# Kernel optimization log

Hardware: AMD Instinct MI355X
Metric: run time of the kernel (lower is better)

Reference implementation:

```python
import jax, jax.numpy as jnp
import numpy as np

B, S, D = 4, 2048, 1024
LN_EPS = 1e-3  # keras LayerNormalization default epsilon


def setup_inputs() -> dict:
    key = jax.random.key(0)
    ks = jax.random.split(key, 6)
    context = jax.random.normal(ks[0], (B, S, D), jnp.float32)
    eos_mask = jax.random.randint(ks[1], (B, 1, S, S), 0, 2).astype(jnp.int32)
    prior = jax.random.uniform(ks[2], (1,), jnp.float32)
    ln_gamma = jnp.ones((D,), jnp.float32)
    ln_beta = jnp.zeros((D,), jnp.float32)
    Wk = jax.random.normal(ks[3], (D, D), jnp.float32) / np.float32(np.sqrt(D))
    bk = jnp.zeros((D,), jnp.float32)
    Wq = jax.random.normal(ks[4], (D, D), jnp.float32) / np.float32(np.sqrt(D))
    bq = jnp.zeros((D,), jnp.float32)
    return dict(context=context, eos_mask=eos_mask, prior=prior,
                ln_gamma=ln_gamma, ln_beta=ln_beta, Wk=Wk, bk=bk, Wq=Wq, bq=bq)


def reference(context, eos_mask, prior, ln_gamma, ln_beta, Wk, bk, Wq, bq):
    seq_len = context.shape[1]
    d_model = jnp.float32(context.shape[-1])
    eos = jnp.squeeze(eos_mask, 1)  # [B,S,S]

    # LayerNorm over last axis
    mu = jnp.mean(context, axis=-1, keepdims=True)
    var = jnp.var(context, axis=-1, keepdims=True)
    x = (context - mu) * jax.lax.rsqrt(var + LN_EPS) * ln_gamma + ln_beta

    # constant band / triangular matrices
    a_mat = jnp.eye(seq_len, k=1, dtype=jnp.float32)
    b_mat = jnp.eye(seq_len, dtype=jnp.float32)
    c_mat = jnp.eye(seq_len, k=-1, dtype=jnp.float32)
    tri = jnp.triu(jnp.ones((seq_len, seq_len), jnp.float32))

    # mask: eos AND (super- or sub-diagonal)
    mask = ((eos != 0) & ((a_mat + c_mat) == 1.0)).astype(jnp.float32)

    k = x @ Wk + bk  # [B,S,D]
    q = x @ Wq + bq  # [B,S,D]
    scores = jnp.einsum('bqd,bkd->bqk', q, k) / d_model + mask * 1e-19
    neibor_attn = jax.nn.softmax(scores, axis=-1)
    neibor_attn = jnp.sqrt(jnp.square(neibor_attn + 1e-9))
    neibor_attn = prior + (1.0 - prior) * neibor_attn  # prior [1] broadcasts

    # log-domain cumulative (triangular) matmuls
    t_mat = jnp.einsum('bij,jk->bik', jnp.log(neibor_attn + 1e-9) * a_mat, tri)
    g_attn = jnp.exp(jnp.einsum('ij,bjk->bik', tri, t_mat)) * (tri - b_mat)
    g_attn = g_attn + jnp.transpose(g_attn, (0, 2, 1)) + (neibor_attn * b_mat + 1e-9)
    return (g_attn, neibor_attn)
```

## Files before the change

kernel.cpp:

```cpp
#include <hip/hip_runtime.h>

#define S_LEN 2048
#define D_MODEL 1024
#define NB 4

typedef unsigned short u16;
typedef __attribute__((ext_vector_type(8))) short short8;
typedef __attribute__((ext_vector_type(4))) float f32x4;
typedef __attribute__((ext_vector_type(4))) unsigned short u16x4;

__device__ inline u16 f2bf(float f) {
  union { float f; unsigned u; } v; v.f = f;
  unsigned u = v.u;
  unsigned r = (u + 0x7FFFu + ((u >> 16) & 1u)) >> 16;
  return (u16)r;
}

__device__ inline float bf2f(u16 b) {
  union { unsigned u; float f; } v; v.u = ((unsigned)b) << 16;
  return v.f;
}

__device__ inline void glds16(const void* g, void* l) {
  __builtin_amdgcn_global_load_lds((const __attribute__((address_space(1))) void*)g,
                                   (__attribute__((address_space(3))) void*)l,
                                   16, 0, 0);
}

__global__ __launch_bounds__(256) void w2_kernel(const float* __restrict__ Wk,
                                                 const float* __restrict__ bq,
                                                 float* __restrict__ w2) {
  const int r = blockIdx.x * 4 + (threadIdx.x >> 6);
  const int lane = threadIdx.x & 63;
  const f32x4* row = (const f32x4*)(Wk + (size_t)r * D_MODEL);
  float s = 0.0f;
  #pragma unroll
  for (int c = 0; c < 4; ++c) {
    const f32x4 v = row[lane * 4 + c];
    const f32x4 b = ((const f32x4*)bq)[lane * 4 + c];
    s += v[0]*b[0] + v[1]*b[1] + v[2]*b[2] + v[3]*b[3];
  }
  for (int o = 32; o > 0; o >>= 1) s += __shfl_xor(s, o);
  if (lane == 0) w2[r] = s;
}

__global__ __launch_bounds__(256) void ln_kernel(const float* __restrict__ ctx,
                                                 const float* __restrict__ gamma,
                                                 const float* __restrict__ beta,
                                                 const float* __restrict__ w2,
                                                 u16* __restrict__ xb,
                                                 float* __restrict__ bvec) {
  const int row = blockIdx.x;
  const int t = threadIdx.x;
  const f32x4 v = ((const f32x4*)(ctx + (size_t)row * D_MODEL))[t];
  float s = v[0] + v[1] + v[2] + v[3];
  float q = v[0]*v[0] + v[1]*v[1] + v[2]*v[2] + v[3]*v[3];
  for (int o = 32; o > 0; o >>= 1) { s += __shfl_xor(s, o); q += __shfl_xor(q, o); }
  __shared__ float rs[4], rq[4], rd[4];
  const int wave = t >> 6, lane = t & 63;
  if (lane == 0) { rs[wave] = s; rq[wave] = q; }
  __syncthreads();
  s = rs[0] + rs[1] + rs[2] + rs[3];
  q = rq[0] + rq[1] + rq[2] + rq[3];
  const float mu = s * (1.0f / D_MODEL);
  const float var = q * (1.0f / D_MODEL) - mu * mu;
  const float rstd = rsqrtf(var + 1e-3f);
  const f32x4 g4 = ((const f32x4*)gamma)[t];
  const f32x4 b4 = ((const f32x4*)beta)[t];
  const f32x4 w4 = ((const f32x4*)w2)[t];
  float xv[4];
  float dot = 0.0f;
  #pragma unroll
  for (int u = 0; u < 4; ++u) {
    xv[u] = (v[u] - mu) * rstd * g4[u] + b4[u];
    dot += xv[u] * w4[u];
  }
  u16x4 o;
  #pragma unroll
  for (int u = 0; u < 4; ++u) o[u] = f2bf(xv[u]);
  ((u16x4*)(xb + (size_t)row * D_MODEL))[t] = o;
  for (int of = 32; of > 0; of >>= 1) dot += __shfl_xor(dot, of);
  if (lane == 0) rd[wave] = dot;
  __syncthreads();
  if (t == 0) bvec[row] = (rd[0] + rd[1] + rd[2] + rd[3]) * (1.0f / D_MODEL);
}

__global__ __launch_bounds__(256) void prep_w(const float* __restrict__ Wq,
                                              const float* __restrict__ Wk,
                                              u16* __restrict__ Wt) {
  __shared__ float tile[32][33];
  const int k0 = blockIdx.x * 32;
  const int n0 = blockIdx.y * 32;
  const int tx = threadIdx.x, ty = threadIdx.y;
  const float* W = (n0 < D_MODEL) ? Wq : Wk;
  const int nl0 = (n0 < D_MODEL) ? n0 : (n0 - D_MODEL);
  #pragma unroll
  for (int j = 0; j < 32; j += 8)
    tile[ty + j][tx] = W[(size_t)(k0 + ty + j) * D_MODEL + nl0 + tx];
  __syncthreads();
  #pragma unroll
  for (int j = 0; j < 32; j += 8)
    Wt[(size_t)(n0 + ty + j) * D_MODEL + k0 + tx] = f2bf(tile[tx][ty + j]);
}

__global__ __launch_bounds__(256, 2) void gemm_bt(
    const u16* __restrict__ A, int lda, long long sA,
    const u16* __restrict__ Bt, int ldb, long long sB,
    u16* __restrict__ C, int ldc, long long sC,
    float scale, int K) {
  __shared__ u16 As[128][32];
  __shared__ u16 Bs[128][32];
  const int tid = threadIdx.x;
  const int wave = tid >> 6, lane = tid & 63;
  const int z = blockIdx.z;
  A += (size_t)z * sA;
  Bt += (size_t)z * sB;
  const size_t m0 = (size_t)blockIdx.y * 128;
  const size_t n0 = (size_t)blockIdx.x * 128;
  const int wr = (wave >> 1) * 64;
  const int wc = (wave & 1) * 64;
  const int strow = wave * 16 + (lane >> 2);
  const int stslot = (lane & 3) * 8;
  const int fr = lane & 15, fq = lane >> 4;

  f32x4 acc[4][4];
  #pragma unroll
  for (int i = 0; i < 4; ++i)
    #pragma unroll
    for (int j = 0; j < 4; ++j) acc[i][j] = (f32x4)(0.0f);

  for (int k0 = 0; k0 < K; k0 += 32) {
    const u16* ga = A + (m0 + strow) * lda + k0 + stslot;
    const u16* gb = Bt + (n0 + strow) * ldb + k0 + stslot;
    glds16(ga, &As[wave * 16][0]);
    glds16(ga + (size_t)64 * lda, &As[64 + wave * 16][0]);
    glds16(gb, &Bs[wave * 16][0]);
    glds16(gb + (size_t)64 * ldb, &Bs[64 + wave * 16][0]);
    __syncthreads();
    short8 af[4], bfv[4];
    #pragma unroll
    for (int mi = 0; mi < 4; ++mi) af[mi] = *(const short8*)&As[wr + mi * 16 + fr][fq * 8];
    #pragma unroll
    for (int ni = 0; ni < 4; ++ni) bfv[ni] = *(const short8*)&Bs[wc + ni * 16 + fr][fq * 8];
    #pragma unroll
    for (int mi = 0; mi < 4; ++mi)
      #pragma unroll
      for (int ni = 0; ni < 4; ++ni)
        acc[mi][ni] = __builtin_amdgcn_mfma_f32_16x16x32_bf16(af[mi], bfv[ni], acc[mi][ni], 0, 0, 0);
    __syncthreads();
  }

  #pragma unroll
  for (int mi = 0; mi < 4; ++mi)
    #pragma unroll
    for (int ni = 0; ni < 4; ++ni) {
      const size_t row = m0 + wr + mi * 16 + fq * 4;
      const size_t col = n0 + wc + ni * 16 + fr;
      #pragma unroll
      for (int r = 0; r < 4; ++r)
        C[((size_t)z * sC) + (row + r) * ldc + col] = f2bf(acc[mi][ni][r] * scale);
    }
}

__global__ __launch_bounds__(512, 2) void gemm8p256(
    const u16* __restrict__ A, int lda, long long sA,
    const u16* __restrict__ Bt, int ldb, long long sB,
    u16* __restrict__ C, int ldc, long long sC,
    float scale, int K) {
  __shared__ char smem[131072];
  const int tid = threadIdx.x;
  const int wave = tid >> 6, lane = tid & 63;
  const int fr = lane & 15, fq = lane >> 4;
  const int wm = wave >> 2, wn = wave & 3;
  const int z = blockIdx.z;
  const size_t m0 = (size_t)blockIdx.y * 256;
  const size_t n0 = (size_t)blockIdx.x * 256;
  const u16* Ab = A + (size_t)z * sA + m0 * lda;
  const u16* Bb = Bt + (size_t)z * sB + n0 * ldb;
  const int perA = (lane >> 3) * lda + (((lane & 7) ^ (lane >> 3)) * 8);
  const int perB = (lane >> 3) * ldb + (((lane & 7) ^ (lane >> 3)) * 8);
  const int u0v = wave * 2, u1v = wave * 2 + 1;
  const int rA_0 = (u0v & 7) * 8 + (u0v >> 3) * 128;
  const int rA_1 = (u1v & 7) * 8 + (u1v >> 3) * 128;
  const int rB_0 = (u0v >> 2) * 64 + (u0v & 3) * 8;
  const int rB_1 = (u1v >> 2) * 64 + (u1v & 3) * 8;
  const int sw0 = ((fq) ^ (fr & 7)) * 16;
  const int sw1 = ((4 + fq) ^ (fr & 7)) * 16;
  const int aBase = wm * 16384 + fr * 128;
  const int bBase = 32768 + wn * 8192 + fr * 128;

  f32x4 acc[8][4];
  #pragma unroll
  for (int i = 0; i < 8; ++i)
    #pragma unroll
    for (int j = 0; j < 4; ++j) acc[i][j] = (f32x4)(0.0f);

#define STG_A02(BUF, KK) do { \
    glds16(Ab + (size_t)rA_0 * lda + perA + (KK), smem + (BUF) + rA_0 * 128); \
    glds16(Ab + (size_t)rA_1 * lda + perA + (KK), smem + (BUF) + rA_1 * 128); } while (0)
#define STG_A13(BUF, KK) do { \
    glds16(Ab + (size_t)(rA_0 + 64) * lda + perA + (KK), smem + (BUF) + (rA_0 + 64) * 128); \
    glds16(Ab + (size_t)(rA_1 + 64) * lda + perA + (KK), smem + (BUF) + (rA_1 + 64) * 128); } while (0)
#define STG_BEV(BUF, KK) do { \
    glds16(Bb + (size_t)rB_0 * ldb + perB + (KK), smem + (BUF) + 32768 + rB_0 * 128); \
    glds16(Bb + (size_t)rB_1 * ldb + perB + (KK), smem + (BUF) + 32768 + rB_1 * 128); } while (0)
#define STG_BOD(BUF, KK) do { \
    glds16(Bb + (size_t)(rB_0 + 32) * ldb + perB + (KK), smem + (BUF) + 32768 + (rB_0 + 32) * 128); \
    glds16(Bb + (size_t)(rB_1 + 32) * ldb + perB + (KK), smem + (BUF) + 32768 + (rB_1 + 32) * 128); } while (0)

  const int NT = K >> 6;
  STG_A02(0, 0); STG_BEV(0, 0); STG_BOD(0, 0); STG_A13(0, 0);

  for (int t = 0; t < NT; ++t) {
    const int bo = (t & 1) * 65536;
    const int bn = bo ^ 65536;
    const int kk = (t + 1 < NT) ? (t + 1) * 64 : 0;
    short8 a0[8], a1[8], be[4], bod[4];

    asm volatile("s_waitcnt vmcnt(4)" ::: "memory");
    asm volatile("s_barrier" ::: "memory");
    #pragma unroll
    for (int fi = 0; fi < 4; ++fi) {
      a0[fi * 2 + 0] = *(const short8*)(smem + bo + aBase + fi * 2048 + sw0);
      a0[fi * 2 + 1] = *(const short8*)(smem + bo + aBase + fi * 2048 + sw1);
    }
    #pragma unroll
    for (int nj = 0; nj < 2; ++nj) {
      be[nj * 2 + 0] = *(const short8*)(smem + bo + bBase + nj * 2048 + sw0);
      be[nj * 2 + 1] = *(const short8*)(smem + bo + bBase + nj * 2048 + sw1);
    }
    STG_A02(bn, kk);
    __builtin_amdgcn_s_setprio(1);
    #pragma unroll
    for (int ks = 0; ks < 2; ++ks)
      #pragma unroll
      for (int fi = 0; fi < 4; ++fi)
        #pragma unroll
        for (int nj = 0; nj < 2; ++nj)
          acc[fi][nj] = __builtin_amdgcn_mfma_f32_16x16x32_bf16(a0[fi * 2 + ks], be[nj * 2 + ks], acc[fi][nj], 0, 0, 0);
    __builtin_amdgcn_s_setprio(0);

    asm volatile("s_waitcnt vmcnt(4)" ::: "memory");
    asm volatile("s_barrier" ::: "memory");
    #pragma unroll
    for (int nj = 0; nj < 2; ++nj) {
      bod[nj * 2 + 0] = *(const short8*)(smem + bo + bBase + 4096 + nj * 2048 + sw0);
      bod[nj * 2 + 1] = *(const short8*)(smem + bo + bBase + 4096 + nj * 2048 + sw1);
    }
    STG_BEV(bn, kk);
    __builtin_amdgcn_s_setprio(1);
    #pragma unroll
    for (int ks = 0; ks < 2; ++ks)
      #pragma unroll
      for (int fi = 0; fi < 4; ++fi)
        #pragma unroll
        for (int nj = 0; nj < 2; ++nj)
          acc[fi][2 + nj] = __builtin_amdgcn_mfma_f32_16x16x32_bf16(a0[fi * 2 + ks], bod[nj * 2 + ks], acc[fi][2 + nj], 0, 0, 0);
    __builtin_amdgcn_s_setprio(0);

    asm volatile("s_waitcnt vmcnt(4)" ::: "memory");
    asm volatile("s_barrier" ::: "memory");
    #pragma unroll
    for (int fi = 0; fi < 4; ++fi) {
      a1[fi * 2 + 0] = *(const short8*)(smem + bo + aBase + 8192 + fi * 2048 + sw0);
      a1[fi * 2 + 1] = *(const short8*)(smem + bo + aBase + 8192 + fi * 2048 + sw1);
    }
    STG_BOD(bn, kk);
    __builtin_amdgcn_s_setprio(1);
    #pragma unroll
    for (int ks = 0; ks < 2; ++ks)
      #pragma unroll
      for (int fi = 0; fi < 4; ++fi)
        #pragma unroll
        for (int nj = 0; nj < 2; ++nj)
          acc[4 + fi][nj] = __builtin_amdgcn_mfma_f32_16x16x32_bf16(a1[fi * 2 + ks], be[nj * 2 + ks], acc[4 + fi][nj], 0, 0, 0);
    __builtin_amdgcn_s_setprio(0);

    asm volatile("s_barrier" ::: "memory");
    STG_A13(bn, kk);
    __builtin_amdgcn_s_setprio(1);
    #pragma unroll
    for (int ks = 0; ks < 2; ++ks)
      #pragma unroll
      for (int fi = 0; fi < 4; ++fi)
        #pragma unroll
        for (int nj = 0; nj < 2; ++nj)
          acc[4 + fi][2 + nj] = __builtin_amdgcn_mfma_f32_16x16x32_bf16(a1[fi * 2 + ks], bod[nj * 2 + ks], acc[4 + fi][2 + nj], 0, 0, 0);
    __builtin_amdgcn_s_setprio(0);
  }
#undef STG_A02
#undef STG_A13
#undef STG_BEV
#undef STG_BOD

  u16* Cz = C + (size_t)z * sC;
  #pragma unroll
  for (int mi = 0; mi < 8; ++mi)
    #pragma unroll
    for (int ni = 0; ni < 4; ++ni) {
      const size_t row = m0 + wm * 128 + (mi >> 2) * 64 + (mi & 3) * 16 + fq * 4;
      const size_t col = n0 + wn * 64 + (ni >> 1) * 32 + (ni & 1) * 16 + fr;
      #pragma unroll
      for (int r = 0; r < 4; ++r)
        Cz[(row + r) * ldc + col] = f2bf(acc[mi][ni][r] * scale);
    }
}

__global__ __launch_bounds__(256) void softmax_kernel(const u16* __restrict__ Sb,
                                                      const float* __restrict__ bvec,
                                                      const float* __restrict__ prior,
                                                      float* __restrict__ na,
                                                      float* __restrict__ ell,
                                                      float* __restrict__ dvec) {
  const int row = blockIdx.x;
  const int t = threadIdx.x;
  const int b = row >> 11, i = row & (S_LEN - 1);
  const short8 sv = ((const short8*)(Sb + (size_t)row * S_LEN))[t];
  const f32x4 bv0 = ((const f32x4*)(bvec + (size_t)b * S_LEN))[t * 2];
  const f32x4 bv1 = ((const f32x4*)(bvec + (size_t)b * S_LEN))[t * 2 + 1];
  float v[8];
  #pragma unroll
  for (int u = 0; u < 8; ++u)
    v[u] = bf2f((u16)sv[u]) + ((u < 4) ? bv0[u] : bv1[u - 4]);
  float mx = v[0];
  #pragma unroll
  for (int u = 1; u < 8; ++u) mx = fmaxf(mx, v[u]);
  for (int o = 32; o > 0; o >>= 1) mx = fmaxf(mx, __shfl_xor(mx, o));
  __shared__ float red[4], red2[4];
  const int wave = t >> 6, lane = t & 63;
  if (lane == 0) red[wave] = mx;
  __syncthreads();
  mx = fmaxf(fmaxf(red[0], red[1]), fmaxf(red[2], red[3]));
  float e[8], s = 0.0f;
  #pragma unroll
  for (int u = 0; u < 8; ++u) { e[u] = __expf(v[u] - mx); s += e[u]; }
  for (int o = 32; o > 0; o >>= 1) s += __shfl_xor(s, o);
  if (lane == 0) red2[wave] = s;
  __syncthreads();
  s = red2[0] + red2[1] + red2[2] + red2[3];
  const float pr = prior[0];
  const float w = 1.0f - pr;
  const float inv = 1.0f / s;
  f32x4 o0, o1;
  #pragma unroll
  for (int u = 0; u < 4; ++u) o0[u] = pr + w * (e[u] * inv + 1e-9f);
  #pragma unroll
  for (int u = 0; u < 4; ++u) o1[u] = pr + w * (e[4 + u] * inv + 1e-9f);
  f32x4* nrow = (f32x4*)(na + (size_t)row * S_LEN);
  nrow[t * 2] = o0;
  nrow[t * 2 + 1] = o1;
  #pragma unroll
  for (int u = 0; u < 8; ++u) {
    const int j = t * 8 + u;
    const float ov = (u < 4) ? o0[u] : o1[u - 4];
    if (j == i) dvec[row] = ov;
    if (j == i + 1) ell[row] = logf(ov + 1e-9f);
  }
  if (i == S_LEN - 1 && t == 0) ell[row] = 0.0f;
}

__global__ __launch_bounds__(256) void scan_kernel(const float* __restrict__ ell,
                                                   float* __restrict__ Cpre) {
  const int b = blockIdx.x, t = threadIdx.x;
  const float* eb = ell + (size_t)b * S_LEN;
  const f32x4 e0 = ((const f32x4*)eb)[t * 2];
  const f32x4 e1 = ((const f32x4*)eb)[t * 2 + 1];
  float ev[8];
  #pragma unroll
  for (int u = 0; u < 4; ++u) ev[u] = e0[u];
  #pragma unroll
  for (int u = 0; u < 4; ++u) ev[4 + u] = e1[u];
  float loc[8], tot = 0.0f;
  #pragma unroll
  for (int u = 0; u < 8; ++u) { loc[u] = tot; tot += ev[u]; }
  __shared__ float sbuf[256];
  sbuf[t] = tot;
  __syncthreads();
  for (int off = 1; off < 256; off <<= 1) {
    const float v = (t >= off) ? sbuf[t - off] : 0.0f;
    __syncthreads();
    sbuf[t] += v;
    __syncthreads();
  }
  const float base = (t == 0) ? 0.0f : sbuf[t - 1];
  #pragma unroll
  for (int u = 0; u < 8; ++u)
    Cpre[(size_t)b * S_LEN + t * 8 + u] = base + loc[u];
}

__global__ __launch_bounds__(256) void gattn_kernel(const float* __restrict__ Cpre,
                                                    const float* __restrict__ dvec,
                                                    float* __restrict__ g) {
  const int b = blockIdx.z, i = blockIdx.y;
  const int j0 = blockIdx.x * 1024 + threadIdx.x * 4;
  const float Ci = Cpre[b * S_LEN + i];
  const float di = dvec[b * S_LEN + i];
  const f32x4 Cj = *(const f32x4*)&Cpre[b * S_LEN + j0];
  f32x4 o;
  #pragma unroll
  for (int u = 0; u < 4; ++u) {
    const int j = j0 + u;
    const float arg = (j > i) ? (Cj[u] - Ci) : (Ci - Cj[u]);
    o[u] = (j == i) ? (di + 1e-9f) : (__expf(arg) + 1e-9f);
  }
  *(f32x4*)(g + ((size_t)b * S_LEN + i) * S_LEN + j0) = o;
}

extern "C" void kernel_launch(void* const* d_in, const int* in_sizes, int n_in,
                              void* d_out, int out_size, void* d_ws, size_t ws_size,
                              hipStream_t stream) {
  const float* ctx   = (const float*)d_in[0];
  const float* prior = (const float*)d_in[2];
  const float* gamma = (const float*)d_in[3];
  const float* beta  = (const float*)d_in[4];
  const float* Wk    = (const float*)d_in[5];
  const float* Wq    = (const float*)d_in[7];
  const float* bq    = (const float*)d_in[8];

  float* g  = (float*)d_out;
  float* na = g + (size_t)NB * S_LEN * S_LEN;

  u16* Xb = (u16*)na;
  u16* Yb = Xb + (size_t)(NB * S_LEN) * D_MODEL;
  u16* PT = Yb + (size_t)(NB * S_LEN) * D_MODEL;
  u16* Wt = PT + (size_t)D_MODEL * D_MODEL;
  u16* Sb = (u16*)g;
  float* w2   = (float*)d_ws;
  float* bvec = w2 + D_MODEL;
  float* ell  = bvec + NB * S_LEN;
  float* dvec = ell + NB * S_LEN;
  float* Cpre = dvec + NB * S_LEN;

  w2_kernel<<<D_MODEL / 4, 256, 0, stream>>>(Wk, bq, w2);
  ln_kernel<<<NB * S_LEN, 256, 0, stream>>>(ctx, gamma, beta, w2, Xb, bvec);
  prep_w<<<dim3(32, 64), dim3(32, 8), 0, stream>>>(Wq, Wk, Wt);

  gemm_bt<<<dim3(8, 8, 1), 256, 0, stream>>>(Wt + (size_t)D_MODEL * D_MODEL, D_MODEL, 0,
                                             Wt, D_MODEL, 0,
                                             PT, D_MODEL, 0, 1.0f, D_MODEL);
  gemm_bt<<<dim3(8, 64, 1), 256, 0, stream>>>(Xb, D_MODEL, 0,
                                              PT, D_MODEL, 0,
                                              Yb, D_MODEL, 0, 1.0f, D_MODEL);
  gemm8p256<<<dim3(8, 8, NB), 512, 0, stream>>>(Yb, D_MODEL, (long long)S_LEN * D_MODEL,
                                                Xb, D_MODEL, (long long)S_LEN * D_MODEL,
                                                Sb, S_LEN, (long long)S_LEN * S_LEN,
                                                1.0f / (float)D_MODEL, D_MODEL);

  softmax_kernel<<<NB * S_LEN, 256, 0, stream>>>(Sb, bvec, prior, na, ell, dvec);
  scan_kernel<<<NB, 256, 0, stream>>>(ell, Cpre);
  gattn_kernel<<<dim3(2, S_LEN, NB), 256, 0, stream>>>(Cpre, dvec, g);
}
```

Baseline: 144.2 us.

## Run batched score GEMM in FP8 via scaled MFMA and tile the projection GEMM

The layer norm kernel now also writes an e4m3 FP8 copy of the normalized activations. The projection GEMM moves to a new 128x256 pipelined kernel that emits FP8 output. The large batched score GEMM becomes a new FP8 kernel built on the 32x32x64 scaled MFMA with 128-wide K steps. The goal is to halve operand bandwidth and raise matrix throughput in the dominant GEMM. The cost is lower precision in the scores, which the softmax and log/exp chain may amplify, and a fully drained vmcnt(0) wait each iteration.

```diff
diff --git a/kernel.cpp b/kernel.cpp
--- a/kernel.cpp
+++ b/kernel.cpp
@@ -1,4 +1,5 @@
 #include <hip/hip_runtime.h>
+#include <hip/hip_fp8.h>
 
 #define S_LEN 2048
 #define D_MODEL 1024
@@ -7,7 +8,10 @@
 typedef unsigned short u16;
 typedef __attribute__((ext_vector_type(8))) short short8;
 typedef __attribute__((ext_vector_type(4))) float f32x4;
+typedef __attribute__((ext_vector_type(16))) float f32x16;
 typedef __attribute__((ext_vector_type(4))) unsigned short u16x4;
+typedef __attribute__((ext_vector_type(4))) int i32x4;
+typedef __attribute__((ext_vector_type(8))) int i32x8;
 
 __device__ inline u16 f2bf(float f) {
   union { float f; unsigned u; } v; v.f = f;
@@ -21,10 +25,22 @@
   return v.f;
 }
 
+__device__ inline unsigned char f2e4m3(float f) {
+  __hip_fp8_e4m3 q(f);
+  return (unsigned char)q.__x;
+}
+
 __device__ inline void glds16(const void* g, void* l) {
   __builtin_amdgcn_global_load_lds((const __attribute__((address_space(1))) void*)g,
                                    (__attribute__((address_space(3))) void*)l,
                                    16, 0, 0);
+}
+
+__device__ inline i32x8 cat8(i32x4 a, i32x4 b) {
+  i32x8 r;
+  r[0] = a[0]; r[1] = a[1]; r[2] = a[2]; r[3] = a[3];
+  r[4] = b[0]; r[5] = b[1]; r[6] = b[2]; r[7] = b[3];
+  return r;
 }
 
 __global__ __launch_bounds__(256) void w2_kernel(const float* __restrict__ Wk,
@@ -49,6 +65,7 @@
                                                  const float* __restrict__ beta,
                                                  const float* __restrict__ w2,
                                                  u16* __restrict__ xb,
+                                                 unsigned char* __restrict__ x8,
                                                  float* __restrict__ bvec) {
   const int row = blockIdx.x;
   const int t = threadIdx.x;
@@ -79,6 +96,9 @@
   #pragma unroll
   for (int u = 0; u < 4; ++u) o[u] = f2bf(xv[u]);
   ((u16x4*)(xb + (size_t)row * D_MODEL))[t] = o;
+  unsigned pk = (unsigned)f2e4m3(xv[0]) | ((unsigned)f2e4m3(xv[1]) << 8) |
+                ((unsigned)f2e4m3(xv[2]) << 16) | ((unsigned)f2e4m3(xv[3]) << 24);
+  ((unsigned*)(x8 + (size_t)row * D_MODEL))[t] = pk;
   for (int of = 32; of > 0; of >>= 1) dot += __shfl_xor(dot, of);
   if (lane == 0) rd[wave] = dot;
   __syncthreads();
@@ -104,17 +124,14 @@
 }
 
 __global__ __launch_bounds__(256, 2) void gemm_bt(
-    const u16* __restrict__ A, int lda, long long sA,
-    const u16* __restrict__ Bt, int ldb, long long sB,
-    u16* __restrict__ C, int ldc, long long sC,
+    const u16* __restrict__ A, int lda,
+    const u16* __restrict__ Bt, int ldb,
+    u16* __restrict__ C, int ldc,
     float scale, int K) {
   __shared__ u16 As[128][32];
   __shared__ u16 Bs[128][32];
   const int tid = threadIdx.x;
   const int wave = tid >> 6, lane = tid & 63;
-  const int z = blockIdx.z;
-  A += (size_t)z * sA;
-  Bt += (size_t)z * sB;
   const size_t m0 = (size_t)blockIdx.y * 128;
   const size_t n0 = (size_t)blockIdx.x * 128;
   const int wr = (wave >> 1) * 64;
@@ -158,151 +175,232 @@
       const size_t col = n0 + wc + ni * 16 + fr;
       #pragma unroll
       for (int r = 0; r < 4; ++r)
-        C[((size_t)z * sC) + (row + r) * ldc + col] = f2bf(acc[mi][ni][r] * scale);
+        C[(row + r) * ldc + col] = f2bf(acc[mi][ni][r] * scale);
     }
 }
 
-__global__ __launch_bounds__(512, 2) void gemm8p256(
-    const u16* __restrict__ A, int lda, long long sA,
-    const u16* __restrict__ Bt, int ldb, long long sB,
+__global__ __launch_bounds__(512, 2) void gemm8p128(
+    const u16* __restrict__ A, int lda,
+    const u16* __restrict__ Bt, int ldb,
+    unsigned char* __restrict__ C8, int ldc,
+    float scale, int K) {
+  __shared__ char smem[98304];
+  const int tid = threadIdx.x;
+  const int wave = tid >> 6, lane = tid & 63;
+  const int fr = lane & 15, fq = lane >> 4;
+  const int wm = wave >> 2, wn = wave & 3;
+  const size_t m0 = (size_t)blockIdx.y * 128;
+  const size_t n0 = (size_t)blockIdx.x * 256;
+  const u16* Ab = A + m0 * lda;
+  const u16* Bb = Bt + n0 * ldb;
+  const int perA = (lane >> 3) * lda + (((lane & 7) ^ (lane >> 3)) * 8);
+  const int perB = (lane >> 3) * ldb + (((lane & 7) ^ (lane >> 3)) * 8);
+  const int u0v = wave * 2, u1v = wave * 2 + 1;
+  const int rA_0 = u0v * 8;
+  const int rA_1 = u1v * 8;
+  const int rB_0 = (u0v >> 2) * 64 + (u0v & 3) * 8;
+  const int rB_1 = (u1v >> 2) * 64 + (u1v & 3) * 8;
+  const int sw0 = ((fq) ^ (fr & 7)) * 16;
+  const int sw1 = ((4 + fq) ^ (fr & 7)) * 16;
+  const int aBase = wm * 8192 + fr * 128;
+  const int bBase = 16384 + wn * 8192 + fr * 128;
+
+  f32x4 acc[4][4];
+  #pragma unroll
+  for (int i = 0; i < 4; ++i)
+    #pragma unroll
+    for (int j = 0; j < 4; ++j) acc[i][j] = (f32x4)(0.0f);
+
+#define STG_A(BUF, KK) do { \
+    glds16(Ab + (size_t)rA_0 * lda + perA + (KK), smem + (BUF) + rA_0 * 128); \
+    glds16(Ab + (size_t)rA_1 * lda + perA + (KK), smem + (BUF) + rA_1 * 128); } while (0)
+#define STG_BEV(BUF, KK) do { \
+    glds16(Bb + (size_t)rB_0 * ldb + perB + (KK), smem + (BUF) + 16384 + rB_0 * 128); \
+    glds16(Bb + (size_t)rB_1 * ldb + perB + (KK), smem + (BUF) + 16384 + rB_1 * 128); } while (0)
+#define STG_BOD(BUF, KK) do { \
+    glds16(Bb + (size_t)(rB_0 + 32) * ldb + perB + (KK), smem + (BUF) + 16384 + (rB_0 + 32) * 128); \
+    glds16(Bb + (size_t)(rB_1 + 32) * ldb + perB + (KK), smem + (BUF) + 16384 + (rB_1 + 32) * 128); } while (0)
+
+  const int NT = K >> 6;
+  STG_A(0, 0); STG_BEV(0, 0); STG_BOD(0, 0);
+
+  for (int t = 0; t < NT; ++t) {
+    const int bo = (t & 1) * 49152;
+    const int bn = bo ^ 49152;
+    const int kk = (t + 1 < NT) ? (t + 1) * 64 : 0;
+    short8 af[8], bv[4];
+
+    asm volatile("s_waitcnt vmcnt(2)" ::: "memory");
+    asm volatile("s_barrier" ::: "memory");
+    #pragma unroll
+    for (int fi = 0; fi < 4; ++fi) {
+      af[fi * 2 + 0] = *(const short8*)(smem + bo + aBase + fi * 2048 + sw0);
+      af[fi * 2 + 1] = *(const short8*)(smem + bo + aBase + fi * 2048 + sw1);
+    }
+    #pragma unroll
+    for (int nj = 0; nj < 2; ++nj) {
+      bv[nj * 2 + 0] = *(const short8*)(smem + bo + bBase + nj * 2048 + sw0);
+      bv[nj * 2 + 1] = *(const short8*)(smem + bo + bBase + nj * 2048 + sw1);
+    }
+    STG_A(bn, kk);
+    STG_BEV(bn, kk);
+    __builtin_amdgcn_s_setprio(1);
+    #pragma unroll
+    for (int ks = 0; ks < 2; ++ks)
+      #pragma unroll
+      for (int fi = 0; fi < 4; ++fi)
+        #pragma unroll
+        for (int nj = 0; nj < 2; ++nj)
+          acc[fi][nj] = __builtin_amdgcn_mfma_f32_16x16x32_bf16(af[fi * 2 + ks], bv[nj * 2 + ks], acc[fi][nj], 0, 0, 0);
+    __builtin_amdgcn_s_setprio(0);
+
+    asm volatile("s_waitcnt vmcnt(4)" ::: "memory");
+    asm volatile("s_barrier" ::: "memory");
+    #pragma unroll
+    for (int nj = 0; nj < 2; ++nj) {
+      bv[nj * 2 + 0] = *(const short8*)(smem + bo + bBase + 4096 + nj * 2048 + sw0);
+      bv[nj * 2 + 1] = *(const short8*)(smem + bo + bBase + 4096 + nj * 2048 + sw1);
+    }
+    STG_BOD(bn, kk);
+    __builtin_amdgcn_s_setprio(1);
+    #pragma unroll
+    for (int ks = 0; ks < 2; ++ks)
+      #pragma unroll
+      for (int fi = 0; fi < 4; ++fi)
+        #pragma unroll
+        for (int nj = 0; nj < 2; ++nj)
+          acc[fi][2 + nj] = __builtin_amdgcn_mfma_f32_16x16x32_bf16(af[fi * 2 + ks], bv[nj * 2 + ks], acc[fi][2 + nj], 0, 0, 0);
+    __builtin_amdgcn_s_setprio(0);
+  }
+#undef STG_A
+#undef STG_BEV
+#undef STG_BOD
+
+  #pragma unroll
+  for (int fi = 0; fi < 4; ++fi)
+    #pragma unroll
+    for (int ni = 0; ni < 4; ++ni) {
+      const size_t row = m0 + wm * 64 + fi * 16 + fq * 4;
+      const size_t col = n0 + wn * 64 + (ni >> 1) * 32 + (ni & 1) * 16 + fr;
+      #pragma unroll
+      for (int r = 0; r < 4; ++r)
+        C8[(row + r) * ldc + col] = f2e4m3(acc[fi][ni][r] * scale);
+    }
+}
+
+__global__ __launch_bounds__(512, 2) void gemm8pF8(
+    const unsigned char* __restrict__ A8, long long sA,
+    const unsigned char* __restrict__ B8, long long sB,
     u16* __restrict__ C, int ldc, long long sC,
     float scale, int K) {
   __shared__ char smem[131072];
   const int tid = threadIdx.x;
   const int wave = tid >> 6, lane = tid & 63;
-  const int fr = lane & 15, fq = lane >> 4;
   const int wm = wave >> 2, wn = wave & 3;
   const int z = blockIdx.z;
   const size_t m0 = (size_t)blockIdx.y * 256;
   const size_t n0 = (size_t)blockIdx.x * 256;
-  const u16* Ab = A + (size_t)z * sA + m0 * lda;
-  const u16* Bb = Bt + (size_t)z * sB + n0 * ldb;
-  const int perA = (lane >> 3) * lda + (((lane & 7) ^ (lane >> 3)) * 8);
-  const int perB = (lane >> 3) * ldb + (((lane & 7) ^ (lane >> 3)) * 8);
-  const int u0v = wave * 2, u1v = wave * 2 + 1;
-  const int rA_0 = (u0v & 7) * 8 + (u0v >> 3) * 128;
-  const int rA_1 = (u1v & 7) * 8 + (u1v >> 3) * 128;
-  const int rB_0 = (u0v >> 2) * 64 + (u0v & 3) * 8;
-  const int rB_1 = (u1v >> 2) * 64 + (u1v & 3) * 8;
-  const int sw0 = ((fq) ^ (fr & 7)) * 16;
-  const int sw1 = ((4 + fq) ^ (fr & 7)) * 16;
-  const int aBase = wm * 16384 + fr * 128;
-  const int bBase = 32768 + wn * 8192 + fr * 128;
-
-  f32x4 acc[8][4];
-  #pragma unroll
-  for (int i = 0; i < 8; ++i)
-    #pragma unroll
-    for (int j = 0; j < 4; ++j) acc[i][j] = (f32x4)(0.0f);
-
-#define STG_A02(BUF, KK) do { \
-    glds16(Ab + (size_t)rA_0 * lda + perA + (KK), smem + (BUF) + rA_0 * 128); \
-    glds16(Ab + (size_t)rA_1 * lda + perA + (KK), smem + (BUF) + rA_1 * 128); } while (0)
-#define STG_A13(BUF, KK) do { \
-    glds16(Ab + (size_t)(rA_0 + 64) * lda + perA + (KK), smem + (BUF) + (rA_0 + 64) * 128); \
-    glds16(Ab + (size_t)(rA_1 + 64) * lda + perA + (KK), smem + (BUF) + (rA_1 + 64) * 128); } while (0)
-#define STG_BEV(BUF, KK) do { \
-    glds16(Bb + (size_t)rB_0 * ldb + perB + (KK), smem + (BUF) + 32768 + rB_0 * 128); \
-    glds16(Bb + (size_t)rB_1 * ldb + perB + (KK), smem + (BUF) + 32768 + rB_1 * 128); } while (0)
-#define STG_BOD(BUF, KK) do { \
-    glds16(Bb + (size_t)(rB_0 + 32) * ldb + perB + (KK), smem + (BUF) + 32768 + (rB_0 + 32) * 128); \
-    glds16(Bb + (size_t)(rB_1 + 32) * ldb + perB + (KK), smem + (BUF) + 32768 + (rB_1 + 32) * 128); } while (0)
-
-  const int NT = K >> 6;
-  STG_A02(0, 0); STG_BEV(0, 0); STG_BOD(0, 0); STG_A13(0, 0);
+  const unsigned char* Ab = A8 + (size_t)z * sA + m0 * K;
+  const unsigned char* Bb = B8 + (size_t)z * sB + n0 * K;
+  const int perL = (lane >> 3) * K + (((lane & 7) ^ (lane >> 3)) * 16);
+  const int w4 = wave * 4;
+  const int r7l = lane & 7;
+  const int hi = lane >> 5;
+  const int l31 = lane & 31;
+  const int swk0_0 = ((hi * 2) ^ r7l) * 16;
+  const int swk0_1 = ((hi * 2 + 1) ^ r7l) * 16;
+  const int swk1_0 = ((4 + hi * 2) ^ r7l) * 16;
+  const int swk1_1 = ((4 + hi * 2 + 1) ^ r7l) * 16;
+  const int aOff = wm * 16384 + l31 * 128;
+  const int bOff = 32768 + wn * 8192 + l31 * 128;
+
+  f32x16 acc[4][2];
+  #pragma unroll
+  for (int i = 0; i < 4; ++i)
+    #pragma unroll
+    for (int j = 0; j < 2; ++j) acc[i][j] = (f32x16)(0.0f);
+
+#define STG_A8(BUF, KK, C0) do { \
+    glds16(Ab + (size_t)((w4 + (C0)) * 8) * K + perL + (KK), smem + (BUF) + (w4 + (C0)) * 1024); \
+    glds16(Ab + (size_t)((w4 + (C0) + 1) * 8) * K + perL + (KK), smem + (BUF) + (w4 + (C0) + 1) * 1024); } while (0)
+#define STG_B8(BUF, KK, C0) do { \
+    glds16(Bb + (size_t)((w4 + (C0)) * 8) * K + perL + (KK), smem + (BUF) + 32768 + (w4 + (C0)) * 1024); \
+    glds16(Bb + (size_t)((w4 + (C0) + 1) * 8) * K + perL + (KK), smem + (BUF) + 32768 + (w4 + (C0) + 1) * 1024); } while (0)
+
+  const int NT = K >> 7;
+  STG_A8(0, 0, 0); STG_A8(0, 0, 2); STG_B8(0, 0, 0); STG_B8(0, 0, 2);
 
   for (int t = 0; t < NT; ++t) {
     const int bo = (t & 1) * 65536;
     const int bn = bo ^ 65536;
-    const int kk = (t + 1 < NT) ? (t + 1) * 64 : 0;
-    short8 a0[8], a1[8], be[4], bod[4];
-
-    asm volatile("s_waitcnt vmcnt(4)" ::: "memory");
+    const int kk = (t + 1 < NT) ? (t + 1) * 128 : 0;
+    i32x8 afr[4], bfr[2];
+
+    asm volatile("s_waitcnt vmcnt(0)" ::: "memory");
     asm volatile("s_barrier" ::: "memory");
     #pragma unroll
-    for (int fi = 0; fi < 4; ++fi) {
-      a0[fi * 2 + 0] = *(const short8*)(smem + bo + aBase + fi * 2048 + sw0);
-      a0[fi * 2 + 1] = *(const short8*)(smem + bo + aBase + fi * 2048 + sw1);
-    }
-    #pragma unroll
-    for (int nj = 0; nj < 2; ++nj) {
-      be[nj * 2 + 0] = *(const short8*)(smem + bo + bBase + nj * 2048 + sw0);
-      be[nj * 2 + 1] = *(const short8*)(smem + bo + bBase + nj * 2048 + sw1);
-    }
-    STG_A02(bn, kk);
+    for (int mt = 0; mt < 4; ++mt)
+      afr[mt] = cat8(*(const i32x4*)(smem + bo + aOff + mt * 4096 + swk0_0),
+                     *(const i32x4*)(smem + bo + aOff + mt * 4096 + swk0_1));
+    bfr[0] = cat8(*(const i32x4*)(smem + bo + bOff + swk0_0),
+                  *(const i32x4*)(smem + bo + bOff + swk0_1));
+    STG_A8(bn, kk, 0); STG_B8(bn, kk, 0);
     __builtin_amdgcn_s_setprio(1);
     #pragma unroll
-    for (int ks = 0; ks < 2; ++ks)
+    for (int mt = 0; mt < 4; ++mt)
+      acc[mt][0] = __builtin_amdgcn_mfma_scale_f32_32x32x64_f8f6f4(
+          afr[mt], bfr[0], acc[mt][0], 0, 0, 0, 0x7F7F7F7F, 0, 0x7F7F7F7F);
+    __builtin_amdgcn_s_setprio(0);
+
+    asm volatile("s_barrier" ::: "memory");
+    bfr[1] = cat8(*(const i32x4*)(smem + bo + bOff + 4096 + swk0_0),
+                  *(const i32x4*)(smem + bo + bOff + 4096 + swk0_1));
+    STG_A8(bn, kk, 2); STG_B8(bn, kk, 2);
+    __builtin_amdgcn_s_setprio(1);
+    #pragma unroll
+    for (int mt = 0; mt < 4; ++mt)
+      acc[mt][1] = __builtin_amdgcn_mfma_scale_f32_32x32x64_f8f6f4(
+          afr[mt], bfr[1], acc[mt][1], 0, 0, 0, 0x7F7F7F7F, 0, 0x7F7F7F7F);
+    __builtin_amdgcn_s_setprio(0);
+
+    asm volatile("s_barrier" ::: "memory");
+    #pragma unroll
+    for (int mt = 0; mt < 4; ++mt)
+      afr[mt] = cat8(*(const i32x4*)(smem + bo + aOff + mt * 4096 + swk1_0),
+                     *(const i32x4*)(smem + bo + aOff + mt * 4096 + swk1_1));
+    bfr[0] = cat8(*(const i32x4*)(smem + bo + bOff + swk1_0),
+                  *(const i32x4*)(smem + bo + bOff + swk1_1));
+    __builtin_amdgcn_s_setprio(1);
+    #pragma unroll
+    for (int mt = 0; mt < 4; ++mt)
+      acc[mt][0] = __builtin_amdgcn_mfma_scale_f32_32x32x64_f8f6f4(
+          afr[mt], bfr[0], acc[mt][0], 0, 0, 0, 0x7F7F7F7F, 0, 0x7F7F7F7F);
+    __builtin_amdgcn_s_setprio(0);
+
+    asm volatile("s_barrier" ::: "memory");
+    bfr[1] = cat8(*(const i32x4*)(smem + bo + bOff + 4096 + swk1_0),
+                  *(const i32x4*)(smem + bo + bOff + 4096 + swk1_1));
+    __builtin_amdgcn_s_setprio(1);
+    #pragma unroll
+    for (int mt = 0; mt < 4; ++mt)
+      acc[mt][1] = __builtin_amdgcn_mfma_scale_f32_32x32x64_f8f6f4(
+          afr[mt], bfr[1], acc[mt][1], 0, 0, 0, 0x7F7F7F7F, 0, 0x7F7F7F7F);
+    __builtin_amdgcn_s_setprio(0);
+  }
+#undef STG_A8
+#undef STG_B8
+
+  u16* Cz = C + (size_t)z * sC;
+  #pragma unroll
+  for (int mt = 0; mt < 4; ++mt)
+    #pragma unroll
+    for (int nt = 0; nt < 2; ++nt) {
+      const size_t colg = n0 + wn * 64 + nt * 32 + l31;
       #pragma unroll
-      for (int fi = 0; fi < 4; ++fi)
-        #pragma unroll
-        for (int nj = 0; nj < 2; ++nj)
-          acc[fi][nj] = __builtin_amdgcn_mfma_f32_16x16x32_bf16(a0[fi * 2 + ks], be[nj * 2 + ks], acc[fi][nj], 0, 0, 0);
-    __builtin_amdgcn_s_setprio(0);
-
-    asm volatile("s_waitcnt vmcnt(4)" ::: "memory");
-    asm volatile("s_barrier" ::: "memory");
-    #pragma unroll
-    for (int nj = 0; nj < 2; ++nj) {
-      bod[nj * 2 + 0] = *(const short8*)(smem + bo + bBase + 4096 + nj * 2048 + sw0);
-      bod[nj * 2 + 1] = *(const short8*)(smem + bo + bBase + 4096 + nj * 2048 + sw1);
-    }
-    STG_BEV(bn, kk);
-    __builtin_amdgcn_s_setprio(1);
-    #pragma unroll
-    for (int ks = 0; ks < 2; ++ks)
-      #pragma unroll
-      for (int fi = 0; fi < 4; ++fi)
-        #pragma unroll
-        for (int nj = 0; nj < 2; ++nj)
-          acc[fi][2 + nj] = __builtin_amdgcn_mfma_f32_16x16x32_bf16(a0[fi * 2 + ks], bod[nj * 2 + ks], acc[fi][2 + nj], 0, 0, 0);
-    __builtin_amdgcn_s_setprio(0);
-
-    asm volatile("s_waitcnt vmcnt(4)" ::: "memory");
-    asm volatile("s_barrier" ::: "memory");
-    #pragma unroll
-    for (int fi = 0; fi < 4; ++fi) {
-      a1[fi * 2 + 0] = *(const short8*)(smem + bo + aBase + 8192 + fi * 2048 + sw0);
-      a1[fi * 2 + 1] = *(const short8*)(smem + bo + aBase + 8192 + fi * 2048 + sw1);
-    }
-    STG_BOD(bn, kk);
-    __builtin_amdgcn_s_setprio(1);
-    #pragma unroll
-    for (int ks = 0; ks < 2; ++ks)
-      #pragma unroll
-      for (int fi = 0; fi < 4; ++fi)
-        #pragma unroll
-        for (int nj = 0; nj < 2; ++nj)
-          acc[4 + fi][nj] = __builtin_amdgcn_mfma_f32_16x16x32_bf16(a1[fi * 2 + ks], be[nj * 2 + ks], acc[4 + fi][nj], 0, 0, 0);
-    __builtin_amdgcn_s_setprio(0);
-
-    asm volatile("s_barrier" ::: "memory");
-    STG_A13(bn, kk);
-    __builtin_amdgcn_s_setprio(1);
-    #pragma unroll
-    for (int ks = 0; ks < 2; ++ks)
-      #pragma unroll
-      for (int fi = 0; fi < 4; ++fi)
-        #pragma unroll
-        for (int nj = 0; nj < 2; ++nj)
-          acc[4 + fi][2 + nj] = __builtin_amdgcn_mfma_f32_16x16x32_bf16(a1[fi * 2 + ks], bod[nj * 2 + ks], acc[4 + fi][2 + nj], 0, 0, 0);
-    __builtin_amdgcn_s_setprio(0);
-  }
-#undef STG_A02
-#undef STG_A13
-#undef STG_BEV
-#undef STG_BOD
-
-  u16* Cz = C + (size_t)z * sC;
-  #pragma unroll
-  for (int mi = 0; mi < 8; ++mi)
-    #pragma unroll
-    for (int ni = 0; ni < 4; ++ni) {
-      const size_t row = m0 + wm * 128 + (mi >> 2) * 64 + (mi & 3) * 16 + fq * 4;
-      const size_t col = n0 + wn * 64 + (ni >> 1) * 32 + (ni & 1) * 16 + fr;
-      #pragma unroll
-      for (int r = 0; r < 4; ++r)
-        Cz[(row + r) * ldc + col] = f2bf(acc[mi][ni][r] * scale);
+      for (int r = 0; r < 16; ++r) {
+        const size_t rowg = m0 + wm * 128 + mt * 32 + (r & 3) + 8 * (r >> 2) + 4 * hi;
+        Cz[rowg * ldc + colg] = f2bf(acc[mt][nt][r] * scale);
+      }
     }
 }
 
@@ -421,8 +519,9 @@
   float* na = g + (size_t)NB * S_LEN * S_LEN;
 
   u16* Xb = (u16*)na;
-  u16* Yb = Xb + (size_t)(NB * S_LEN) * D_MODEL;
-  u16* PT = Yb + (size_t)(NB * S_LEN) * D_MODEL;
+  unsigned char* X8 = (unsigned char*)(Xb + (size_t)(NB * S_LEN) * D_MODEL);
+  unsigned char* Y8 = X8 + (size_t)(NB * S_LEN) * D_MODEL;
+  u16* PT = (u16*)(Y8 + (size_t)(NB * S_LEN) * D_MODEL);
   u16* Wt = PT + (size_t)D_MODEL * D_MODEL;
   u16* Sb = (u16*)g;
   float* w2   = (float*)d_ws;
@@ -432,19 +531,19 @@
   float* Cpre = dvec + NB * S_LEN;
 
   w2_kernel<<<D_MODEL / 4, 256, 0, stream>>>(Wk, bq, w2);
-  ln_kernel<<<NB * S_LEN, 256, 0, stream>>>(ctx, gamma, beta, w2, Xb, bvec);
+  ln_kernel<<<NB * S_LEN, 256, 0, stream>>>(ctx, gamma, beta, w2, Xb, X8, bvec);
   prep_w<<<dim3(32, 64), dim3(32, 8), 0, stream>>>(Wq, Wk, Wt);
 
-  gemm_bt<<<dim3(8, 8, 1), 256, 0, stream>>>(Wt + (size_t)D_MODEL * D_MODEL, D_MODEL, 0,
-                                             Wt, D_MODEL, 0,
-                                             PT, D_MODEL, 0, 1.0f, D_MODEL);
-  gemm_bt<<<dim3(8, 64, 1), 256, 0, stream>>>(Xb, D_MODEL, 0,
-                                              PT, D_MODEL, 0,
-                                              Yb, D_MODEL, 0, 1.0f, D_MODEL);
-  gemm8p256<<<dim3(8, 8, NB), 512, 0, stream>>>(Yb, D_MODEL, (long long)S_LEN * D_MODEL,
-                                                Xb, D_MODEL, (long long)S_LEN * D_MODEL,
-                                                Sb, S_LEN, (long long)S_LEN * S_LEN,
-                                                1.0f / (float)D_MODEL, D_MODEL);
+  gemm_bt<<<dim3(8, 8, 1), 256, 0, stream>>>(Wt + (size_t)D_MODEL * D_MODEL, D_MODEL,
+                                             Wt, D_MODEL,
+                                             PT, D_MODEL, 1.0f, D_MODEL);
+  gemm8p128<<<dim3(4, 64, 1), 512, 0, stream>>>(Xb, D_MODEL,
+                                                PT, D_MODEL,
+                                                Y8, D_MODEL, 1.0f, D_MODEL);
+  gemm8pF8<<<dim3(8, 8, NB), 512, 0, stream>>>(Y8, (long long)S_LEN * D_MODEL,
+                                               X8, (long long)S_LEN * D_MODEL,
+                                               Sb, S_LEN, (long long)S_LEN * S_LEN,
+                                               1.0f / (float)D_MODEL, D_MODEL);
 
   softmax_kernel<<<NB * S_LEN, 256, 0, stream>>>(Sb, bvec, prior, na, ell, dvec);
   scan_kernel<<<NB, 256, 0, stream>>>(ell, Cpre);
```

Result: faster. 123.8 us (-14.2%).
